# Kernel tuning notes

Hardware: AMD Instinct MI355X
Metric: run time of the kernel (lower is better)

## Reference

```python
import jax, jax.numpy as jnp
import numpy as np

N, D_IN, D_HID, D_OUT, E, STEPS = 50000, 64, 64, 32, 800000, 3


def setup_inputs() -> dict:
    key = jax.random.key(0)
    ks = jax.random.split(key, 8)
    x = jax.random.normal(ks[0], (N, D_IN), dtype=jnp.float32)
    edge_index = jax.random.randint(ks[1], (2, E), 0, N, dtype=jnp.int32)
    s1 = 1.0 / np.sqrt(2 * D_IN)
    s2 = 1.0 / np.sqrt(D_IN)
    s3 = 1.0 / np.sqrt(2 * D_HID)
    s4 = 1.0 / np.sqrt(D_HID)
    W_att1 = jax.random.uniform(ks[2], (2 * D_IN, 1), jnp.float32, -s1, s1)
    b_att1 = jax.random.uniform(ks[3], (1,), jnp.float32, -s1, s1)
    W_lin1 = jax.random.uniform(ks[4], (D_IN, D_HID), jnp.float32, -s2, s2)
    W_att2 = jax.random.uniform(ks[5], (2 * D_HID, 1), jnp.float32, -s3, s3)
    b_att2 = jax.random.uniform(ks[6], (1,), jnp.float32, -s3, s3)
    W_lin2 = jax.random.uniform(ks[7], (D_HID, D_OUT), jnp.float32, -s4, s4)
    return {"x": x, "edge_index": edge_index, "W_att1": W_att1, "b_att1": b_att1,
            "W_lin1": W_lin1, "W_att2": W_att2, "b_att2": b_att2, "W_lin2": W_lin2}


def _aggregate_mean(h, src, dst, n):
    # mean over incoming neighbors; nodes with no in-edges get 0 (clamped denom)
    feat_sum = jax.ops.segment_sum(h[src], dst, num_segments=n)
    deg = jax.ops.segment_sum(jnp.ones_like(src, dtype=h.dtype), dst, num_segments=n)
    return feat_sum / jnp.maximum(deg, 1.0)[:, None]


def _gcn_conv(x, src, dst, W_att, b_att, W_lin, n):
    h_src = x[src]                       # [E, d]
    h_dst = x[dst]                       # [E, d]
    score = jax.nn.leaky_relu(
        jnp.concatenate([h_src, h_dst], axis=-1) @ W_att + b_att)  # [E, 1]
    weighted = score * (h_src @ W_lin)   # [E, d_out]
    feats = jax.ops.segment_sum(weighted, dst, num_segments=n)
    att = jax.ops.segment_sum(jnp.abs(weighted), dst, num_segments=n)
    return feats, att


def reference(x, edge_index, W_att1, b_att1, W_lin1, W_att2, b_att2, W_lin2):
    src, dst = edge_index[0], edge_index[1]
    n = x.shape[0]
    # graphSmoothing positional encoding: stack of [x, mean^1(x), ..., mean^S(x)], then mean over steps
    h = x
    acc = x
    for _ in range(STEPS):
        h = _aggregate_mean(h, src, dst, n)
        acc = acc + h
    xs = acc / (STEPS + 1)
    h1, _att1 = _gcn_conv(xs, src, dst, W_att1, b_att1, W_lin1, n)
    h1 = jax.nn.relu(h1)  # dropout is identity in eval mode
    out, _att2 = _gcn_conv(h1, src, dst, W_att2, b_att2, W_lin2, n)
    # y=None -> loss_separation = loss_focus = 0
    return out
```

## Files before the change

kernel.cpp:

```cpp
#include <hip/hip_runtime.h>


typedef __attribute__((ext_vector_type(8))) _Float16 half8;
typedef __attribute__((ext_vector_type(4))) _Float16 half4v;
typedef __attribute__((ext_vector_type(2))) _Float16 half2v;

#define CHUNK 1024

#define UNPACK8(iraw, ss)                                                     \
    ss[0] = (iraw).x & 0xffffu; ss[1] = (iraw).x >> 16;                       \
    ss[2] = (iraw).y & 0xffffu; ss[3] = (iraw).y >> 16;                       \
    ss[4] = (iraw).z & 0xffffu; ss[5] = (iraw).z >> 16;                       \
    ss[6] = (iraw).w & 0xffffu; ss[7] = (iraw).w >> 16;

__global__ void binA_kernel(const int* __restrict__ src, const int* __restrict__ dst,
                            unsigned int* __restrict__ packed, int* __restrict__ offs,
                            const float* __restrict__ x, _Float16* __restrict__ x16,
                            int total8, int E) {
    __shared__ int cnt[256];
    __shared__ int pref[256];
    __shared__ int cur[256];
    __shared__ unsigned int stage[CHUNK];
    int t = threadIdx.x;
    int base = blockIdx.x * CHUNK;
    int len = E - base; if (len > CHUNK) len = CHUNK;
    cnt[t] = 0;
    __syncthreads();
    for (int i = t; i < len; i += 256) atomicAdd(&cnt[dst[base + i] >> 8], 1);
    __syncthreads();
    int v = cnt[t];
    pref[t] = v;
    __syncthreads();
    for (int off = 1; off < 256; off <<= 1) {
        int u = (t >= off) ? pref[t - off] : 0;
        __syncthreads();
        pref[t] += u;
        __syncthreads();
    }
    int excl = pref[t] - v;
    cur[t] = excl;
    offs[blockIdx.x * 257 + t] = excl;
    if (t == 255) offs[blockIdx.x * 257 + 256] = pref[255];
    __syncthreads();
    for (int i = t; i < len; i += 256) {
        int s = src[base + i], d = dst[base + i];
        int pos = atomicAdd(&cur[d >> 8], 1);
        stage[pos] = (unsigned int)s | ((unsigned int)d << 16);
    }
    __syncthreads();
    for (int i = t; i < len; i += 256) packed[base + i] = stage[i];
    for (int i = blockIdx.x * 256 + t; i < total8; i += gridDim.x * 256) {
        float4 v0 = ((const float4*)x)[2 * i];
        float4 v1 = ((const float4*)x)[2 * i + 1];
        half8 o;
        o[0] = (_Float16)v0.x; o[1] = (_Float16)v0.y; o[2] = (_Float16)v0.z; o[3] = (_Float16)v0.w;
        o[4] = (_Float16)v1.x; o[5] = (_Float16)v1.y; o[6] = (_Float16)v1.z; o[7] = (_Float16)v1.w;
        ((half8*)x16)[i] = o;
    }
}

__global__ void binB_kernel(const unsigned int* __restrict__ packed,
                            const int* __restrict__ offs,
                            int* __restrict__ deg,
                            unsigned short* __restrict__ src_idx,
                            int nChunks, int N) {
    __shared__ int cnt[256];
    int t = threadIdx.x;
    int p = blockIdx.x;
    if (t < 256) cnt[t] = 0;
    __syncthreads();
    size_t winBase = (size_t)p * 256 * 64;
    for (int c = t; c < nChunks; c += 512) {
        const int* oc = offs + c * 257;
        int o0 = oc[p], o1 = oc[p + 1];
        const unsigned int* pk = packed + (size_t)c * CHUNK;
        for (int i = o0; i < o1; ++i) {
            unsigned int pr = pk[i];
            int ln = (pr >> 16) & 255;
            int slot = atomicAdd(&cnt[ln], 1);
            if (slot < 64)
                src_idx[winBase + (size_t)ln * 64 + slot] = (unsigned short)(pr & 0xffffu);
        }
    }
    __syncthreads();
    if (t < 256) {
        int node = p * 256 + t;
        if (node < N) {
            int d = cnt[t];
            deg[node] = d < 64 ? d : 64;
        }
    }
}

__global__ void agg_mean8_kernel(const _Float16* __restrict__ h,
                                 const int* __restrict__ degp,
                                 const unsigned short* __restrict__ src_idx,
                                 _Float16* __restrict__ h_out, int N) {
    int wid = (blockIdx.x * blockDim.x + threadIdx.x) >> 6;
    int lane = threadIdx.x & 63;
    int node = wid * 2 + (lane >> 5);
    if (node >= N) return;
    int lane32 = lane & 31;
    int beg = node << 6;
    int j = lane32 >> 3, f = lane32 & 7;
    int base = beg + 8 * j;
    uint4 iraw0 = *(const uint4*)(src_idx + base);
    int dgr = degp[node];
    int end = beg + dgr;
    const uint4* rowp = (const uint4*)h;
    float acc[8];
    #pragma unroll
    for (int q = 0; q < 8; ++q) acc[q] = 0.f;
    if (base < end) {
        int ss[8];
        UNPACK8(iraw0, ss)
        #pragma unroll
        for (int k = 0; k < 8; ++k) {
            int e = base + k;
            int s = e < end ? ss[k] : ss[0];
            uint4 raw = rowp[(size_t)s * 8 + f];
            if (e >= end) { raw.x = 0u; raw.y = 0u; raw.z = 0u; raw.w = 0u; }
            half8 v = *(half8*)&raw;
            #pragma unroll
            for (int q = 0; q < 8; ++q) acc[q] += (float)v[q];
        }
    }
    int base1 = base + 32;
    if (base1 < end) {
        uint4 iraw1 = *(const uint4*)(src_idx + base1);
        int ss[8];
        UNPACK8(iraw1, ss)
        #pragma unroll
        for (int k = 0; k < 8; ++k) {
            int e = base1 + k;
            int s = e < end ? ss[k] : ss[0];
            uint4 raw = rowp[(size_t)s * 8 + f];
            if (e >= end) { raw.x = 0u; raw.y = 0u; raw.z = 0u; raw.w = 0u; }
            half8 v = *(half8*)&raw;
            #pragma unroll
            for (int q = 0; q < 8; ++q) acc[q] += (float)v[q];
        }
    }
    #pragma unroll
    for (int q = 0; q < 8; ++q) {
        acc[q] += __shfl_down(acc[q], 16, 64);
        acc[q] += __shfl_down(acc[q], 8, 64);
    }
    if (lane32 < 8) {
        float inv = dgr > 0 ? 1.f / (float)dgr : 0.f;
        half8 o;
        #pragma unroll
        for (int q = 0; q < 8; ++q) o[q] = (_Float16)(acc[q] * inv);
        *((half8*)h_out + (size_t)node * 8 + lane32) = o;
    }
}

__global__ void mean3_xf1_kernel(const _Float16* __restrict__ h ,
                                 const _Float16* __restrict__ x16,
                                 const _Float16* __restrict__ hA ,
                                 const int* __restrict__ degp,
                                 const unsigned short* __restrict__ src_idx,
                                 const float* __restrict__ W_lin1,
                                 const float* __restrict__ W_att1,
                                 _Float16* __restrict__ z1, float* __restrict__ a1,
                                 float* __restrict__ a2, int N) {
    __shared__ float Wl[64 * 64];
    __shared__ float Wa[128];
    __shared__ float rows[4][2][64];
    for (int i = threadIdx.x; i < 1024; i += 256)
        ((float4*)Wl)[i] = ((const float4*)W_lin1)[i];
    if (threadIdx.x < 128) Wa[threadIdx.x] = W_att1[threadIdx.x];
    __syncthreads();
    int w = threadIdx.x >> 6;
    int wid = (blockIdx.x * blockDim.x + threadIdx.x) >> 6;
    int lane = threadIdx.x & 63;
    int halfsel = lane >> 5;
    int node = wid * 2 + halfsel;
    if (node >= N) return;
    int lane32 = lane & 31;
    int beg = node << 6;
    int j = lane32 >> 3, f = lane32 & 7;
    int base = beg + 8 * j;
    uint4 iraw0 = *(const uint4*)(src_idx + base);
    int dgr = degp[node];
    int end = beg + dgr;
    const uint4* rowp = (const uint4*)h;
    float acc[8];
    #pragma unroll
    for (int q = 0; q < 8; ++q) acc[q] = 0.f;
    if (base < end) {
        int ss[8];
        UNPACK8(iraw0, ss)
        #pragma unroll
        for (int k = 0; k < 8; ++k) {
            int e = base + k;
            int s = e < end ? ss[k] : ss[0];
            uint4 raw = rowp[(size_t)s * 8 + f];
            if (e >= end) { raw.x = 0u; raw.y = 0u; raw.z = 0u; raw.w = 0u; }
            half8 v = *(half8*)&raw;
            #pragma unroll
            for (int q = 0; q < 8; ++q) acc[q] += (float)v[q];
        }
    }
    int base1 = base + 32;
    if (base1 < end) {
        uint4 iraw1 = *(const uint4*)(src_idx + base1);
        int ss[8];
        UNPACK8(iraw1, ss)
        #pragma unroll
        for (int k = 0; k < 8; ++k) {
            int e = base1 + k;
            int s = e < end ? ss[k] : ss[0];
            uint4 raw = rowp[(size_t)s * 8 + f];
            if (e >= end) { raw.x = 0u; raw.y = 0u; raw.z = 0u; raw.w = 0u; }
            half8 v = *(half8*)&raw;
            #pragma unroll
            for (int q = 0; q < 8; ++q) acc[q] += (float)v[q];
        }
    }
    #pragma unroll
    for (int q = 0; q < 8; ++q) {
        acc[q] += __shfl_down(acc[q], 16, 64);
        acc[q] += __shfl_down(acc[q], 8, 64);
    }
    float p1 = 0.f, p2 = 0.f;
    if (lane32 < 8) {
        float inv = dgr > 0 ? 1.f / (float)dgr : 0.f;
        half8 xv = *((const half8*)x16 + (size_t)node * 8 + f);
        half8 h1v = *((const half8*)hA + (size_t)node * 8 + f);
        half8 h2v = *((const half8*)h + (size_t)node * 8 + f);
        float xs[8];
        #pragma unroll
        for (int q = 0; q < 8; ++q) {
            xs[q] = ((float)xv[q] + (float)h1v[q] + (float)h2v[q] + acc[q] * inv) * 0.25f;
            p1 += xs[q] * Wa[f * 8 + q];
            p2 += xs[q] * Wa[64 + f * 8 + q];
        }
        *(float4*)&rows[w][halfsel][f * 8]     = make_float4(xs[0], xs[1], xs[2], xs[3]);
        *(float4*)&rows[w][halfsel][f * 8 + 4] = make_float4(xs[4], xs[5], xs[6], xs[7]);
    }
    p1 += __shfl_down(p1, 4, 64); p2 += __shfl_down(p2, 4, 64);
    p1 += __shfl_down(p1, 2, 64); p2 += __shfl_down(p2, 2, 64);
    p1 += __shfl_down(p1, 1, 64); p2 += __shfl_down(p2, 1, 64);
    if (lane32 == 0) { a1[node] = p1; a2[node] = p2; }
    float z0 = 0.f, zb = 0.f;
    const float4* myrow4 = (const float4*)rows[w][halfsel];
    #pragma unroll
    for (int k4 = 0; k4 < 16; ++k4) {
        float4 xk = myrow4[k4];
        float2 w0 = *(const float2*)&Wl[(4 * k4 + 0) * 64 + 2 * lane32];
        float2 w1 = *(const float2*)&Wl[(4 * k4 + 1) * 64 + 2 * lane32];
        float2 w2 = *(const float2*)&Wl[(4 * k4 + 2) * 64 + 2 * lane32];
        float2 w3 = *(const float2*)&Wl[(4 * k4 + 3) * 64 + 2 * lane32];
        z0 += xk.x * w0.x + xk.y * w1.x + xk.z * w2.x + xk.w * w3.x;
        zb += xk.x * w0.y + xk.y * w1.y + xk.z * w2.y + xk.w * w3.y;
    }
    half2v o2; o2.x = (_Float16)z0; o2.y = (_Float16)zb;
    *((half2v*)(z1 + (size_t)node * 64 + 2 * lane32)) = o2;
}

__global__ void conv64_xf2_kernel(const _Float16* __restrict__ z, const float* __restrict__ a1v,
                                  const float* __restrict__ a2v, const float* __restrict__ b_att,
                                  const int* __restrict__ degp,
                                  const unsigned short* __restrict__ src_idx,
                                  const float* __restrict__ W_lin2,
                                  const float* __restrict__ W_att2,
                                  _Float16* __restrict__ z2, float* __restrict__ a1o,
                                  float* __restrict__ a2o, int N) {
    __shared__ float Wl[64 * 32];
    __shared__ float Wa[128];
    __shared__ float rows[4][2][64];
    for (int i = threadIdx.x; i < 512; i += 256)
        ((float4*)Wl)[i] = ((const float4*)W_lin2)[i];
    if (threadIdx.x < 128) Wa[threadIdx.x] = W_att2[threadIdx.x];
    __syncthreads();
    int w = threadIdx.x >> 6;
    int wid = (blockIdx.x * blockDim.x + threadIdx.x) >> 6;
    int lane = threadIdx.x & 63;
    int halfsel = lane >> 5;
    int node = wid * 2 + halfsel;
    if (node >= N) return;
    int lane32 = lane & 31;
    int beg = node << 6;
    int j = lane32 >> 3, f = lane32 & 7;
    int base = beg + 8 * j;
    uint4 iraw0 = *(const uint4*)(src_idx + base);
    float ad = a2v[node] + b_att[0];
    int dgr = degp[node];
    int end = beg + dgr;
    const uint4* rowp = (const uint4*)z;
    float acc[8];
    #pragma unroll
    for (int q = 0; q < 8; ++q) acc[q] = 0.f;
    if (base < end) {
        int ss[8];
        UNPACK8(iraw0, ss)
        #pragma unroll
        for (int k = 0; k < 8; ++k) {
            int e = base + k;
            int s = e < end ? ss[k] : ss[0];
            float sc = a1v[s] + ad;
            sc = sc > 0.f ? sc : 0.01f * sc;
            uint4 raw = rowp[(size_t)s * 8 + f];
            if (e >= end) { raw.x = 0u; raw.y = 0u; raw.z = 0u; raw.w = 0u; }
            half8 v = *(half8*)&raw;
            #pragma unroll
            for (int q = 0; q < 8; ++q) acc[q] += sc * (float)v[q];
        }
    }
    int base1 = base + 32;
    if (base1 < end) {
        uint4 iraw1 = *(const uint4*)(src_idx + base1);
        int ss[8];
        UNPACK8(iraw1, ss)
        #pragma unroll
        for (int k = 0; k < 8; ++k) {
            int e = base1 + k;
            int s = e < end ? ss[k] : ss[0];
            float sc = a1v[s] + ad;
            sc = sc > 0.f ? sc : 0.01f * sc;
            uint4 raw = rowp[(size_t)s * 8 + f];
            if (e >= end) { raw.x = 0u; raw.y = 0u; raw.z = 0u; raw.w = 0u; }
            half8 v = *(half8*)&raw;
            #pragma unroll
            for (int q = 0; q < 8; ++q) acc[q] += sc * (float)v[q];
        }
    }
    #pragma unroll
    for (int q = 0; q < 8; ++q) {
        acc[q] += __shfl_down(acc[q], 16, 64);
        acc[q] += __shfl_down(acc[q], 8, 64);
    }
    float p1 = 0.f, p2 = 0.f;
    if (lane32 < 8) {
        float hreg[8];
        #pragma unroll
        for (int q = 0; q < 8; ++q) {
            hreg[q] = fmaxf(acc[q], 0.f);
            p1 += hreg[q] * Wa[f * 8 + q];
            p2 += hreg[q] * Wa[64 + f * 8 + q];
        }
        *(float4*)&rows[w][halfsel][f * 8]     = make_float4(hreg[0], hreg[1], hreg[2], hreg[3]);
        *(float4*)&rows[w][halfsel][f * 8 + 4] = make_float4(hreg[4], hreg[5], hreg[6], hreg[7]);
    }
    p1 += __shfl_down(p1, 4, 64); p2 += __shfl_down(p2, 4, 64);
    p1 += __shfl_down(p1, 2, 64); p2 += __shfl_down(p2, 2, 64);
    p1 += __shfl_down(p1, 1, 64); p2 += __shfl_down(p2, 1, 64);
    if (lane32 == 0) { a1o[node] = p1; a2o[node] = p2; }
    float zacc = 0.f;
    const float4* myrow4 = (const float4*)rows[w][halfsel];
    #pragma unroll
    for (int k4 = 0; k4 < 16; ++k4) {
        float4 hk = myrow4[k4];
        zacc += hk.x * Wl[(4 * k4 + 0) * 32 + lane32];
        zacc += hk.y * Wl[(4 * k4 + 1) * 32 + lane32];
        zacc += hk.z * Wl[(4 * k4 + 2) * 32 + lane32];
        zacc += hk.w * Wl[(4 * k4 + 3) * 32 + lane32];
    }
    z2[(size_t)node * 32 + lane32] = (_Float16)zacc;
}

__global__ void agg_conv32_kernel(const _Float16* __restrict__ z, const float* __restrict__ a1v,
                                  const float* __restrict__ a2v, const float* __restrict__ b_att,
                                  const int* __restrict__ degp,
                                  const unsigned short* __restrict__ src_idx,
                                  float* __restrict__ outp, int N) {
    int wid = (blockIdx.x * blockDim.x + threadIdx.x) >> 6;
    int lane = threadIdx.x & 63;
    int node = wid * 2 + (lane >> 5);
    if (node >= N) return;
    int lane32 = lane & 31;
    int beg = node << 6;
    int j = lane32 >> 3, f = lane32 & 7;
    int base = beg + 8 * j;
    uint4 iraw0 = *(const uint4*)(src_idx + base);
    float ad = a2v[node] + b_att[0];
    int dgr = degp[node];
    int end = beg + dgr;
    const uint2* rowp = (const uint2*)z;
    float ax = 0.f, ay = 0.f, az = 0.f, aw = 0.f;
    if (base < end) {
        int ss[8];
        UNPACK8(iraw0, ss)
        #pragma unroll
        for (int k = 0; k < 8; ++k) {
            int e = base + k;
            int s = e < end ? ss[k] : ss[0];
            float sc = a1v[s] + ad;
            sc = sc > 0.f ? sc : 0.01f * sc;
            uint2 raw = rowp[(size_t)s * 8 + f];
            if (e >= end) { raw.x = 0u; raw.y = 0u; }
            half4v v = *(half4v*)&raw;
            ax += sc * (float)v[0]; ay += sc * (float)v[1];
            az += sc * (float)v[2]; aw += sc * (float)v[3];
        }
    }
    int base1 = base + 32;
    if (base1 < end) {
        uint4 iraw1 = *(const uint4*)(src_idx + base1);
        int ss[8];
        UNPACK8(iraw1, ss)
        #pragma unroll
        for (int k = 0; k < 8; ++k) {
            int e = base1 + k;
            int s = e < end ? ss[k] : ss[0];
            float sc = a1v[s] + ad;
            sc = sc > 0.f ? sc : 0.01f * sc;
            uint2 raw = rowp[(size_t)s * 8 + f];
            if (e >= end) { raw.x = 0u; raw.y = 0u; }
            half4v v = *(half4v*)&raw;
            ax += sc * (float)v[0]; ay += sc * (float)v[1];
            az += sc * (float)v[2]; aw += sc * (float)v[3];
        }
    }
    ax += __shfl_down(ax, 16, 64); ay += __shfl_down(ay, 16, 64);
    az += __shfl_down(az, 16, 64); aw += __shfl_down(aw, 16, 64);
    ax += __shfl_down(ax, 8, 64);  ay += __shfl_down(ay, 8, 64);
    az += __shfl_down(az, 8, 64);  aw += __shfl_down(aw, 8, 64);
    if (lane32 < 8) {
        float4 o; o.x = ax; o.y = ay; o.z = az; o.w = aw;
        *((float4*)(outp + (size_t)node * 32) + lane32) = o;
    }
}

extern "C" void kernel_launch(void* const* d_in, const int* in_sizes, int n_in,
                              void* d_out, int out_size, void* d_ws, size_t ws_size,
                              hipStream_t stream) {
    const float* x      = (const float*)d_in[0];
    const int*   ei     = (const int*)d_in[1];
    const float* W_att1 = (const float*)d_in[2];
    const float* b_att1 = (const float*)d_in[3];
    const float* W_lin1 = (const float*)d_in[4];
    const float* W_att2 = (const float*)d_in[5];
    const float* b_att2 = (const float*)d_in[6];
    const float* W_lin2 = (const float*)d_in[7];
    float* out = (float*)d_out;

    int N = in_sizes[0] / 64;
    int E = in_sizes[1] / 2;
    const int* src = ei;
    const int* dst = ei + E;
    int nChunks = (E + CHUNK - 1) / CHUNK;
    int nPart   = (N + 255) >> 8;

    char* ws = (char*)d_ws;
    size_t off = 0;
    auto alloc = [&](size_t bytes) -> void* {
        void* p = ws + off;
        off += (bytes + 255) & ~(size_t)255;
        return p;
    };
    int*            deg     = (int*)alloc((size_t)N * 4);
    unsigned short* src_idx = (unsigned short*)alloc((size_t)nPart * 256 * 64 * 2);
    unsigned int*   packed  = (unsigned int*)alloc((size_t)nChunks * CHUNK * 4);
    int*            offs    = (int*)alloc((size_t)nChunks * 257 * 4);
    _Float16* x16 = (_Float16*)alloc((size_t)N * 64 * 2);
    _Float16* hA  = (_Float16*)alloc((size_t)N * 64 * 2);
    _Float16* hB  = (_Float16*)alloc((size_t)N * 64 * 2);
    _Float16* z1  = (_Float16*)alloc((size_t)N * 64 * 2);
    _Float16* z2  = (_Float16*)alloc((size_t)N * 32 * 2);
    float* a1  = (float*)alloc((size_t)N * 4);
    float* a2  = (float*)alloc((size_t)N * 4);
    float* a1b = (float*)alloc((size_t)N * 4);
    float* a2b = (float*)alloc((size_t)N * 4);

    const int tb = 256;
    int total8 = N * 8;

    binA_kernel<<<nChunks, 256, 0, stream>>>(src, dst, packed, offs, x, x16, total8, E);
    binB_kernel<<<nPart, 512, 0, stream>>>(packed, offs, deg, src_idx, nChunks, N);

    int gBlocks = (N + 7) / 8;
    agg_mean8_kernel<<<gBlocks, tb, 0, stream>>>(x16, deg, src_idx, hA, N);
    agg_mean8_kernel<<<gBlocks, tb, 0, stream>>>(hA,  deg, src_idx, hB, N);
    mean3_xf1_kernel<<<gBlocks, tb, 0, stream>>>(hB, x16, hA, deg, src_idx,
                                                 W_lin1, W_att1, z1, a1, a2, N);
    conv64_xf2_kernel<<<gBlocks, tb, 0, stream>>>(z1, a1, a2, b_att1, deg, src_idx,
                                                  W_lin2, W_att2, z2, a1b, a2b, N);
    agg_conv32_kernel<<<gBlocks, tb, 0, stream>>>(z2, a1b, a2b, b_att2, deg, src_idx,
                                                  out, N);
}
```

Baseline: 196.2 us.

## Fuse five aggregation stages into one cooperative persistent kernel with grid syncs

Replaces the five back-to-back per-stage kernel launches with a single cooperative persistent kernel. It grid-strides over node pairs and separates the stages with grid.sync(), reloading the shared-memory weights between conv stages. The stage bodies are factored into device functions shared with the fallback path. The aim is to remove launch gaps and tail effects between small kernels. In exchange, occupancy is capped by the cooperative grid size, and each grid barrier adds its own cost.

After: 476.4 us. +142.8%, slower.

```diff
diff --git a/kernel.cpp b/kernel.cpp
--- a/kernel.cpp
+++ b/kernel.cpp
@@ -1,4 +1,7 @@
 #include <hip/hip_runtime.h>
+#include <hip/hip_cooperative_groups.h>
+
+namespace cg = cooperative_groups;
 
 
 typedef __attribute__((ext_vector_type(8))) _Float16 half8;
@@ -92,6 +95,294 @@
     }
 }
 
+
+__device__ __forceinline__ void agg_mean_body(
+    const _Float16* __restrict__ h, _Float16* __restrict__ h_out,
+    const int* __restrict__ degp, const unsigned short* __restrict__ src_idx,
+    int node, int lane32, int j, int f) {
+    int beg = node << 6;
+    int base = beg + 8 * j;
+    uint4 iraw0 = *(const uint4*)(src_idx + base);
+    int dgr = degp[node];
+    int end = beg + dgr;
+    const uint4* rowp = (const uint4*)h;
+    float acc[8];
+    #pragma unroll
+    for (int q = 0; q < 8; ++q) acc[q] = 0.f;
+    if (base < end) {
+        int ss[8];
+        UNPACK8(iraw0, ss)
+        #pragma unroll
+        for (int k = 0; k < 8; ++k) {
+            int e = base + k;
+            int s = e < end ? ss[k] : ss[0];
+            uint4 raw = rowp[(size_t)s * 8 + f];
+            if (e >= end) { raw.x = 0u; raw.y = 0u; raw.z = 0u; raw.w = 0u; }
+            half8 v = *(half8*)&raw;
+            #pragma unroll
+            for (int q = 0; q < 8; ++q) acc[q] += (float)v[q];
+        }
+    }
+    int base1 = base + 32;
+    if (base1 < end) {
+        uint4 iraw1 = *(const uint4*)(src_idx + base1);
+        int ss[8];
+        UNPACK8(iraw1, ss)
+        #pragma unroll
+        for (int k = 0; k < 8; ++k) {
+            int e = base1 + k;
+            int s = e < end ? ss[k] : ss[0];
+            uint4 raw = rowp[(size_t)s * 8 + f];
+            if (e >= end) { raw.x = 0u; raw.y = 0u; raw.z = 0u; raw.w = 0u; }
+            half8 v = *(half8*)&raw;
+            #pragma unroll
+            for (int q = 0; q < 8; ++q) acc[q] += (float)v[q];
+        }
+    }
+    #pragma unroll
+    for (int q = 0; q < 8; ++q) {
+        acc[q] += __shfl_down(acc[q], 16, 64);
+        acc[q] += __shfl_down(acc[q], 8, 64);
+    }
+    if (lane32 < 8) {
+        float inv = dgr > 0 ? 1.f / (float)dgr : 0.f;
+        half8 o;
+        #pragma unroll
+        for (int q = 0; q < 8; ++q) o[q] = (_Float16)(acc[q] * inv);
+        *((half8*)h_out + (size_t)node * 8 + lane32) = o;
+    }
+}
+
+__device__ __forceinline__ void mean3_xf1_body(
+    const _Float16* __restrict__ h, const _Float16* __restrict__ x16,
+    const _Float16* __restrict__ hA,
+    const int* __restrict__ degp, const unsigned short* __restrict__ src_idx,
+    const float* Wl, const float* Wa, float* myrow,
+    _Float16* __restrict__ z1, float* __restrict__ a1, float* __restrict__ a2,
+    int node, int lane32, int j, int f) {
+    int beg = node << 6;
+    int base = beg + 8 * j;
+    uint4 iraw0 = *(const uint4*)(src_idx + base);
+    int dgr = degp[node];
+    int end = beg + dgr;
+    const uint4* rowp = (const uint4*)h;
+    float acc[8];
+    #pragma unroll
+    for (int q = 0; q < 8; ++q) acc[q] = 0.f;
+    if (base < end) {
+        int ss[8];
+        UNPACK8(iraw0, ss)
+        #pragma unroll
+        for (int k = 0; k < 8; ++k) {
+            int e = base + k;
+            int s = e < end ? ss[k] : ss[0];
+            uint4 raw = rowp[(size_t)s * 8 + f];
+            if (e >= end) { raw.x = 0u; raw.y = 0u; raw.z = 0u; raw.w = 0u; }
+            half8 v = *(half8*)&raw;
+            #pragma unroll
+            for (int q = 0; q < 8; ++q) acc[q] += (float)v[q];
+        }
+    }
+    int base1 = base + 32;
+    if (base1 < end) {
+        uint4 iraw1 = *(const uint4*)(src_idx + base1);
+        int ss[8];
+        UNPACK8(iraw1, ss)
+        #pragma unroll
+        for (int k = 0; k < 8; ++k) {
+            int e = base1 + k;
+            int s = e < end ? ss[k] : ss[0];
+            uint4 raw = rowp[(size_t)s * 8 + f];
+            if (e >= end) { raw.x = 0u; raw.y = 0u; raw.z = 0u; raw.w = 0u; }
+            half8 v = *(half8*)&raw;
+            #pragma unroll
+            for (int q = 0; q < 8; ++q) acc[q] += (float)v[q];
+        }
+    }
+    #pragma unroll
+    for (int q = 0; q < 8; ++q) {
+        acc[q] += __shfl_down(acc[q], 16, 64);
+        acc[q] += __shfl_down(acc[q], 8, 64);
+    }
+    float p1 = 0.f, p2 = 0.f;
+    if (lane32 < 8) {
+        float inv = dgr > 0 ? 1.f / (float)dgr : 0.f;
+        half8 xv = *((const half8*)x16 + (size_t)node * 8 + f);
+        half8 h1v = *((const half8*)hA + (size_t)node * 8 + f);
+        half8 h2v = *((const half8*)h + (size_t)node * 8 + f);
+        float xs[8];
+        #pragma unroll
+        for (int q = 0; q < 8; ++q) {
+            xs[q] = ((float)xv[q] + (float)h1v[q] + (float)h2v[q] + acc[q] * inv) * 0.25f;
+            p1 += xs[q] * Wa[f * 8 + q];
+            p2 += xs[q] * Wa[64 + f * 8 + q];
+        }
+        *(float4*)&myrow[f * 8]     = make_float4(xs[0], xs[1], xs[2], xs[3]);
+        *(float4*)&myrow[f * 8 + 4] = make_float4(xs[4], xs[5], xs[6], xs[7]);
+    }
+    p1 += __shfl_down(p1, 4, 64); p2 += __shfl_down(p2, 4, 64);
+    p1 += __shfl_down(p1, 2, 64); p2 += __shfl_down(p2, 2, 64);
+    p1 += __shfl_down(p1, 1, 64); p2 += __shfl_down(p2, 1, 64);
+    if (lane32 == 0) { a1[node] = p1; a2[node] = p2; }
+    float z0 = 0.f, zb = 0.f;
+    const float4* myrow4 = (const float4*)myrow;
+    #pragma unroll
+    for (int k4 = 0; k4 < 16; ++k4) {
+        float4 xk = myrow4[k4];
+        float2 w0 = *(const float2*)&Wl[(4 * k4 + 0) * 64 + 2 * lane32];
+        float2 w1 = *(const float2*)&Wl[(4 * k4 + 1) * 64 + 2 * lane32];
+        float2 w2 = *(const float2*)&Wl[(4 * k4 + 2) * 64 + 2 * lane32];
+        float2 w3 = *(const float2*)&Wl[(4 * k4 + 3) * 64 + 2 * lane32];
+        z0 += xk.x * w0.x + xk.y * w1.x + xk.z * w2.x + xk.w * w3.x;
+        zb += xk.x * w0.y + xk.y * w1.y + xk.z * w2.y + xk.w * w3.y;
+    }
+    half2v o2; o2.x = (_Float16)z0; o2.y = (_Float16)zb;
+    *((half2v*)(z1 + (size_t)node * 64 + 2 * lane32)) = o2;
+}
+
+__device__ __forceinline__ void conv64_xf2_body(
+    const _Float16* __restrict__ z, const float* __restrict__ a1v,
+    const float* __restrict__ a2v, const float* __restrict__ b_att,
+    const int* __restrict__ degp, const unsigned short* __restrict__ src_idx,
+    const float* Wl, const float* Wa, float* myrow,
+    _Float16* __restrict__ z2, float* __restrict__ a1o, float* __restrict__ a2o,
+    int node, int lane32, int j, int f) {
+    int beg = node << 6;
+    int base = beg + 8 * j;
+    uint4 iraw0 = *(const uint4*)(src_idx + base);
+    float ad = a2v[node] + b_att[0];
+    int dgr = degp[node];
+    int end = beg + dgr;
+    const uint4* rowp = (const uint4*)z;
+    float acc[8];
+    #pragma unroll
+    for (int q = 0; q < 8; ++q) acc[q] = 0.f;
+    if (base < end) {
+        int ss[8];
+        UNPACK8(iraw0, ss)
+        #pragma unroll
+        for (int k = 0; k < 8; ++k) {
+            int e = base + k;
+            int s = e < end ? ss[k] : ss[0];
+            float sc = a1v[s] + ad;
+            sc = sc > 0.f ? sc : 0.01f * sc;
+            uint4 raw = rowp[(size_t)s * 8 + f];
+            if (e >= end) { raw.x = 0u; raw.y = 0u; raw.z = 0u; raw.w = 0u; }
+            half8 v = *(half8*)&raw;
+            #pragma unroll
+            for (int q = 0; q < 8; ++q) acc[q] += sc * (float)v[q];
+        }
+    }
+    int base1 = base + 32;
+    if (base1 < end) {
+        uint4 iraw1 = *(const uint4*)(src_idx + base1);
+        int ss[8];
+        UNPACK8(iraw1, ss)
+        #pragma unroll
+        for (int k = 0; k < 8; ++k) {
+            int e = base1 + k;
+            int s = e < end ? ss[k] : ss[0];
+            float sc = a1v[s] + ad;
+            sc = sc > 0.f ? sc : 0.01f * sc;
+            uint4 raw = rowp[(size_t)s * 8 + f];
+            if (e >= end) { raw.x = 0u; raw.y = 0u; raw.z = 0u; raw.w = 0u; }
+            half8 v = *(half8*)&raw;
+            #pragma unroll
+            for (int q = 0; q < 8; ++q) acc[q] += sc * (float)v[q];
+        }
+    }
+    #pragma unroll
+    for (int q = 0; q < 8; ++q) {
+        acc[q] += __shfl_down(acc[q], 16, 64);
+        acc[q] += __shfl_down(acc[q], 8, 64);
+    }
+    float p1 = 0.f, p2 = 0.f;
+    if (lane32 < 8) {
+        float hreg[8];
+        #pragma unroll
+        for (int q = 0; q < 8; ++q) {
+            hreg[q] = fmaxf(acc[q], 0.f);
+            p1 += hreg[q] * Wa[f * 8 + q];
+            p2 += hreg[q] * Wa[64 + f * 8 + q];
+        }
+        *(float4*)&myrow[f * 8]     = make_float4(hreg[0], hreg[1], hreg[2], hreg[3]);
+        *(float4*)&myrow[f * 8 + 4] = make_float4(hreg[4], hreg[5], hreg[6], hreg[7]);
+    }
+    p1 += __shfl_down(p1, 4, 64); p2 += __shfl_down(p2, 4, 64);
+    p1 += __shfl_down(p1, 2, 64); p2 += __shfl_down(p2, 2, 64);
+    p1 += __shfl_down(p1, 1, 64); p2 += __shfl_down(p2, 1, 64);
+    if (lane32 == 0) { a1o[node] = p1; a2o[node] = p2; }
+    float zacc = 0.f;
+    const float4* myrow4 = (const float4*)myrow;
+    #pragma unroll
+    for (int k4 = 0; k4 < 16; ++k4) {
+        float4 hk = myrow4[k4];
+        zacc += hk.x * Wl[(4 * k4 + 0) * 32 + lane32];
+        zacc += hk.y * Wl[(4 * k4 + 1) * 32 + lane32];
+        zacc += hk.z * Wl[(4 * k4 + 2) * 32 + lane32];
+        zacc += hk.w * Wl[(4 * k4 + 3) * 32 + lane32];
+    }
+    z2[(size_t)node * 32 + lane32] = (_Float16)zacc;
+}
+
+__device__ __forceinline__ void agg_conv32_body(
+    const _Float16* __restrict__ z, const float* __restrict__ a1v,
+    const float* __restrict__ a2v, const float* __restrict__ b_att,
+    const int* __restrict__ degp, const unsigned short* __restrict__ src_idx,
+    float* __restrict__ outp, int node, int lane32, int j, int f) {
+    int beg = node << 6;
+    int base = beg + 8 * j;
+    uint4 iraw0 = *(const uint4*)(src_idx + base);
+    float ad = a2v[node] + b_att[0];
+    int dgr = degp[node];
+    int end = beg + dgr;
+    const uint2* rowp = (const uint2*)z;
+    float ax = 0.f, ay = 0.f, az = 0.f, aw = 0.f;
+    if (base < end) {
+        int ss[8];
+        UNPACK8(iraw0, ss)
+        #pragma unroll
+        for (int k = 0; k < 8; ++k) {
+            int e = base + k;
+            int s = e < end ? ss[k] : ss[0];
+            float sc = a1v[s] + ad;
+            sc = sc > 0.f ? sc : 0.01f * sc;
+            uint2 raw = rowp[(size_t)s * 8 + f];
+            if (e >= end) { raw.x = 0u; raw.y = 0u; }
+            half4v v = *(half4v*)&raw;
+            ax += sc * (float)v[0]; ay += sc * (float)v[1];
+            az += sc * (float)v[2]; aw += sc * (float)v[3];
+        }
+    }
+    int base1 = base + 32;
+    if (base1 < end) {
+        uint4 iraw1 = *(const uint4*)(src_idx + base1);
+        int ss[8];
+        UNPACK8(iraw1, ss)
+        #pragma unroll
+        for (int k = 0; k < 8; ++k) {
+            int e = base1 + k;
+            int s = e < end ? ss[k] : ss[0];
+            float sc = a1v[s] + ad;
+            sc = sc > 0.f ? sc : 0.01f * sc;
+            uint2 raw = rowp[(size_t)s * 8 + f];
+            if (e >= end) { raw.x = 0u; raw.y = 0u; }
+            half4v v = *(half4v*)&raw;
+            ax += sc * (float)v[0]; ay += sc * (float)v[1];
+            az += sc * (float)v[2]; aw += sc * (float)v[3];
+        }
+    }
+    ax += __shfl_down(ax, 16, 64); ay += __shfl_down(ay, 16, 64);
+    az += __shfl_down(az, 16, 64); aw += __shfl_down(aw, 16, 64);
+    ax += __shfl_down(ax, 8, 64);  ay += __shfl_down(ay, 8, 64);
+    az += __shfl_down(az, 8, 64);  aw += __shfl_down(aw, 8, 64);
+    if (lane32 < 8) {
+        float4 o; o.x = ax; o.y = ay; o.z = az; o.w = aw;
+        *((float4*)(outp + (size_t)node * 32) + lane32) = o;
+    }
+}
+
+
 __global__ void agg_mean8_kernel(const _Float16* __restrict__ h,
                                  const int* __restrict__ degp,
                                  const unsigned short* __restrict__ src_idx,
@@ -101,63 +392,12 @@
     int node = wid * 2 + (lane >> 5);
     if (node >= N) return;
     int lane32 = lane & 31;
-    int beg = node << 6;
-    int j = lane32 >> 3, f = lane32 & 7;
-    int base = beg + 8 * j;
-    uint4 iraw0 = *(const uint4*)(src_idx + base);
-    int dgr = degp[node];
-    int end = beg + dgr;
-    const uint4* rowp = (const uint4*)h;
-    float acc[8];
-    #pragma unroll
-    for (int q = 0; q < 8; ++q) acc[q] = 0.f;
-    if (base < end) {
-        int ss[8];
-        UNPACK8(iraw0, ss)
-        #pragma unroll
-        for (int k = 0; k < 8; ++k) {
-            int e = base + k;
-            int s = e < end ? ss[k] : ss[0];
-            uint4 raw = rowp[(size_t)s * 8 + f];
-            if (e >= end) { raw.x = 0u; raw.y = 0u; raw.z = 0u; raw.w = 0u; }
-            half8 v = *(half8*)&raw;
-            #pragma unroll
-            for (int q = 0; q < 8; ++q) acc[q] += (float)v[q];
-        }
-    }
-    int base1 = base + 32;
-    if (base1 < end) {
-        uint4 iraw1 = *(const uint4*)(src_idx + base1);
-        int ss[8];
-        UNPACK8(iraw1, ss)
-        #pragma unroll
-        for (int k = 0; k < 8; ++k) {
-            int e = base1 + k;
-            int s = e < end ? ss[k] : ss[0];
-            uint4 raw = rowp[(size_t)s * 8 + f];
-            if (e >= end) { raw.x = 0u; raw.y = 0u; raw.z = 0u; raw.w = 0u; }
-            half8 v = *(half8*)&raw;
-            #pragma unroll
-            for (int q = 0; q < 8; ++q) acc[q] += (float)v[q];
-        }
-    }
-    #pragma unroll
-    for (int q = 0; q < 8; ++q) {
-        acc[q] += __shfl_down(acc[q], 16, 64);
-        acc[q] += __shfl_down(acc[q], 8, 64);
-    }
-    if (lane32 < 8) {
-        float inv = dgr > 0 ? 1.f / (float)dgr : 0.f;
-        half8 o;
-        #pragma unroll
-        for (int q = 0; q < 8; ++q) o[q] = (_Float16)(acc[q] * inv);
-        *((half8*)h_out + (size_t)node * 8 + lane32) = o;
-    }
-}
-
-__global__ void mean3_xf1_kernel(const _Float16* __restrict__ h ,
+    agg_mean_body(h, h_out, degp, src_idx, node, lane32, lane32 >> 3, lane32 & 7);
+}
+
+__global__ void mean3_xf1_kernel(const _Float16* __restrict__ h,
                                  const _Float16* __restrict__ x16,
-                                 const _Float16* __restrict__ hA ,
+                                 const _Float16* __restrict__ hA,
                                  const int* __restrict__ degp,
                                  const unsigned short* __restrict__ src_idx,
                                  const float* __restrict__ W_lin1,
@@ -178,85 +418,8 @@
     int node = wid * 2 + halfsel;
     if (node >= N) return;
     int lane32 = lane & 31;
-    int beg = node << 6;
-    int j = lane32 >> 3, f = lane32 & 7;
-    int base = beg + 8 * j;
-    uint4 iraw0 = *(const uint4*)(src_idx + base);
-    int dgr = degp[node];
-    int end = beg + dgr;
-    const uint4* rowp = (const uint4*)h;
-    float acc[8];
-    #pragma unroll
-    for (int q = 0; q < 8; ++q) acc[q] = 0.f;
-    if (base < end) {
-        int ss[8];
-        UNPACK8(iraw0, ss)
-        #pragma unroll
-        for (int k = 0; k < 8; ++k) {
-            int e = base + k;
-            int s = e < end ? ss[k] : ss[0];
-            uint4 raw = rowp[(size_t)s * 8 + f];
-            if (e >= end) { raw.x = 0u; raw.y = 0u; raw.z = 0u; raw.w = 0u; }
-            half8 v = *(half8*)&raw;
-            #pragma unroll
-            for (int q = 0; q < 8; ++q) acc[q] += (float)v[q];
-        }
-    }
-    int base1 = base + 32;
-    if (base1 < end) {
-        uint4 iraw1 = *(const uint4*)(src_idx + base1);
-        int ss[8];
-        UNPACK8(iraw1, ss)
-        #pragma unroll
-        for (int k = 0; k < 8; ++k) {
-            int e = base1 + k;
-            int s = e < end ? ss[k] : ss[0];
-            uint4 raw = rowp[(size_t)s * 8 + f];
-            if (e >= end) { raw.x = 0u; raw.y = 0u; raw.z = 0u; raw.w = 0u; }
-            half8 v = *(half8*)&raw;
-            #pragma unroll
-            for (int q = 0; q < 8; ++q) acc[q] += (float)v[q];
-        }
-    }
-    #pragma unroll
-    for (int q = 0; q < 8; ++q) {
-        acc[q] += __shfl_down(acc[q], 16, 64);
-        acc[q] += __shfl_down(acc[q], 8, 64);
-    }
-    float p1 = 0.f, p2 = 0.f;
-    if (lane32 < 8) {
-        float inv = dgr > 0 ? 1.f / (float)dgr : 0.f;
-        half8 xv = *((const half8*)x16 + (size_t)node * 8 + f);
-        half8 h1v = *((const half8*)hA + (size_t)node * 8 + f);
-        half8 h2v = *((const half8*)h + (size_t)node * 8 + f);
-        float xs[8];
-        #pragma unroll
-        for (int q = 0; q < 8; ++q) {
-            xs[q] = ((float)xv[q] + (float)h1v[q] + (float)h2v[q] + acc[q] * inv) * 0.25f;
-            p1 += xs[q] * Wa[f * 8 + q];
-            p2 += xs[q] * Wa[64 + f * 8 + q];
-        }
-        *(float4*)&rows[w][halfsel][f * 8]     = make_float4(xs[0], xs[1], xs[2], xs[3]);
-        *(float4*)&rows[w][halfsel][f * 8 + 4] = make_float4(xs[4], xs[5], xs[6], xs[7]);
-    }
-    p1 += __shfl_down(p1, 4, 64); p2 += __shfl_down(p2, 4, 64);
-    p1 += __shfl_down(p1, 2, 64); p2 += __shfl_down(p2, 2, 64);
-    p1 += __shfl_down(p1, 1, 64); p2 += __shfl_down(p2, 1, 64);
-    if (lane32 == 0) { a1[node] = p1; a2[node] = p2; }
-    float z0 = 0.f, zb = 0.f;
-    const float4* myrow4 = (const float4*)rows[w][halfsel];
-    #pragma unroll
-    for (int k4 = 0; k4 < 16; ++k4) {
-        float4 xk = myrow4[k4];
-        float2 w0 = *(const float2*)&Wl[(4 * k4 + 0) * 64 + 2 * lane32];
-        float2 w1 = *(const float2*)&Wl[(4 * k4 + 1) * 64 + 2 * lane32];
-        float2 w2 = *(const float2*)&Wl[(4 * k4 + 2) * 64 + 2 * lane32];
-        float2 w3 = *(const float2*)&Wl[(4 * k4 + 3) * 64 + 2 * lane32];
-        z0 += xk.x * w0.x + xk.y * w1.x + xk.z * w2.x + xk.w * w3.x;
-        zb += xk.x * w0.y + xk.y * w1.y + xk.z * w2.y + xk.w * w3.y;
-    }
-    half2v o2; o2.x = (_Float16)z0; o2.y = (_Float16)zb;
-    *((half2v*)(z1 + (size_t)node * 64 + 2 * lane32)) = o2;
+    mean3_xf1_body(h, x16, hA, degp, src_idx, Wl, Wa, rows[w][halfsel],
+                   z1, a1, a2, node, lane32, lane32 >> 3, lane32 & 7);
 }
 
 __global__ void conv64_xf2_kernel(const _Float16* __restrict__ z, const float* __restrict__ a1v,
@@ -281,83 +444,8 @@
     int node = wid * 2 + halfsel;
     if (node >= N) return;
     int lane32 = lane & 31;
-    int beg = node << 6;
-    int j = lane32 >> 3, f = lane32 & 7;
-    int base = beg + 8 * j;
-    uint4 iraw0 = *(const uint4*)(src_idx + base);
-    float ad = a2v[node] + b_att[0];
-    int dgr = degp[node];
-    int end = beg + dgr;
-    const uint4* rowp = (const uint4*)z;
-    float acc[8];
-    #pragma unroll
-    for (int q = 0; q < 8; ++q) acc[q] = 0.f;
-    if (base < end) {
-        int ss[8];
-        UNPACK8(iraw0, ss)
-        #pragma unroll
-        for (int k = 0; k < 8; ++k) {
-            int e = base + k;
-            int s = e < end ? ss[k] : ss[0];
-            float sc = a1v[s] + ad;
-            sc = sc > 0.f ? sc : 0.01f * sc;
-            uint4 raw = rowp[(size_t)s * 8 + f];
-            if (e >= end) { raw.x = 0u; raw.y = 0u; raw.z = 0u; raw.w = 0u; }
-            half8 v = *(half8*)&raw;
-            #pragma unroll
-            for (int q = 0; q < 8; ++q) acc[q] += sc * (float)v[q];
-        }
-    }
-    int base1 = base + 32;
-    if (base1 < end) {
-        uint4 iraw1 = *(const uint4*)(src_idx + base1);
-        int ss[8];
-        UNPACK8(iraw1, ss)
-        #pragma unroll
-        for (int k = 0; k < 8; ++k) {
-            int e = base1 + k;
-            int s = e < end ? ss[k] : ss[0];
-            float sc = a1v[s] + ad;
-            sc = sc > 0.f ? sc : 0.01f * sc;
-            uint4 raw = rowp[(size_t)s * 8 + f];
-            if (e >= end) { raw.x = 0u; raw.y = 0u; raw.z = 0u; raw.w = 0u; }
-            half8 v = *(half8*)&raw;
-            #pragma unroll
-            for (int q = 0; q < 8; ++q) acc[q] += sc * (float)v[q];
-        }
-    }
-    #pragma unroll
-    for (int q = 0; q < 8; ++q) {
-        acc[q] += __shfl_down(acc[q], 16, 64);
-        acc[q] += __shfl_down(acc[q], 8, 64);
-    }
-    float p1 = 0.f, p2 = 0.f;
-    if (lane32 < 8) {
-        float hreg[8];
-        #pragma unroll
-        for (int q = 0; q < 8; ++q) {
-            hreg[q] = fmaxf(acc[q], 0.f);
-            p1 += hreg[q] * Wa[f * 8 + q];
-            p2 += hreg[q] * Wa[64 + f * 8 + q];
-        }
-        *(float4*)&rows[w][halfsel][f * 8]     = make_float4(hreg[0], hreg[1], hreg[2], hreg[3]);
-        *(float4*)&rows[w][halfsel][f * 8 + 4] = make_float4(hreg[4], hreg[5], hreg[6], hreg[7]);
-    }
-    p1 += __shfl_down(p1, 4, 64); p2 += __shfl_down(p2, 4, 64);
-    p1 += __shfl_down(p1, 2, 64); p2 += __shfl_down(p2, 2, 64);
-    p1 += __shfl_down(p1, 1, 64); p2 += __shfl_down(p2, 1, 64);
-    if (lane32 == 0) { a1o[node] = p1; a2o[node] = p2; }
-    float zacc = 0.f;
-    const float4* myrow4 = (const float4*)rows[w][halfsel];
-    #pragma unroll
-    for (int k4 = 0; k4 < 16; ++k4) {
-        float4 hk = myrow4[k4];
-        zacc += hk.x * Wl[(4 * k4 + 0) * 32 + lane32];
-        zacc += hk.y * Wl[(4 * k4 + 1) * 32 + lane32];
-        zacc += hk.z * Wl[(4 * k4 + 2) * 32 + lane32];
-        zacc += hk.w * Wl[(4 * k4 + 3) * 32 + lane32];
-    }
-    z2[(size_t)node * 32 + lane32] = (_Float16)zacc;
+    conv64_xf2_body(z, a1v, a2v, b_att, degp, src_idx, Wl, Wa, rows[w][halfsel],
+                    z2, a1o, a2o, node, lane32, lane32 >> 3, lane32 & 7);
 }
 
 __global__ void agg_conv32_kernel(const _Float16* __restrict__ z, const float* __restrict__ a1v,
@@ -370,56 +458,68 @@
     int node = wid * 2 + (lane >> 5);
     if (node >= N) return;
     int lane32 = lane & 31;
-    int beg = node << 6;
+    agg_conv32_body(z, a1v, a2v, b_att, degp, src_idx, outp,
+                    node, lane32, lane32 >> 3, lane32 & 7);
+}
+
+__global__ void fused5_kernel(
+    const _Float16* __restrict__ x16, _Float16* __restrict__ hA,
+    _Float16* __restrict__ hB,
+    const int* __restrict__ degp, const unsigned short* __restrict__ src_idx,
+    const float* __restrict__ W_lin1, const float* __restrict__ W_att1,
+    const float* __restrict__ W_lin2, const float* __restrict__ W_att2,
+    const float* __restrict__ b_att1, const float* __restrict__ b_att2,
+    _Float16* __restrict__ z1, _Float16* __restrict__ z2,
+    float* __restrict__ a1, float* __restrict__ a2,
+    float* __restrict__ a1b, float* __restrict__ a2b,
+    float* __restrict__ outp, int N) {
+    cg::grid_group grid = cg::this_grid();
+    __shared__ float Wl[64 * 64];
+    __shared__ float Wa[128];
+    __shared__ float rows[4][2][64];
+    int t = threadIdx.x;
+    int w = t >> 6;
+    int lane = t & 63;
+    int halfsel = lane >> 5;
+    int lane32 = lane & 31;
     int j = lane32 >> 3, f = lane32 & 7;
-    int base = beg + 8 * j;
-    uint4 iraw0 = *(const uint4*)(src_idx + base);
-    float ad = a2v[node] + b_att[0];
-    int dgr = degp[node];
-    int end = beg + dgr;
-    const uint2* rowp = (const uint2*)z;
-    float ax = 0.f, ay = 0.f, az = 0.f, aw = 0.f;
-    if (base < end) {
-        int ss[8];
-        UNPACK8(iraw0, ss)
-        #pragma unroll
-        for (int k = 0; k < 8; ++k) {
-            int e = base + k;
-            int s = e < end ? ss[k] : ss[0];
-            float sc = a1v[s] + ad;
-            sc = sc > 0.f ? sc : 0.01f * sc;
-            uint2 raw = rowp[(size_t)s * 8 + f];
-            if (e >= end) { raw.x = 0u; raw.y = 0u; }
-            half4v v = *(half4v*)&raw;
-            ax += sc * (float)v[0]; ay += sc * (float)v[1];
-            az += sc * (float)v[2]; aw += sc * (float)v[3];
-        }
-    }
-    int base1 = base + 32;
-    if (base1 < end) {
-        uint4 iraw1 = *(const uint4*)(src_idx + base1);
-        int ss[8];
-        UNPACK8(iraw1, ss)
-        #pragma unroll
-        for (int k = 0; k < 8; ++k) {
-            int e = base1 + k;
-            int s = e < end ? ss[k] : ss[0];
-            float sc = a1v[s] + ad;
-            sc = sc > 0.f ? sc : 0.01f * sc;
-            uint2 raw = rowp[(size_t)s * 8 + f];
-            if (e >= end) { raw.x = 0u; raw.y = 0u; }
-            half4v v = *(half4v*)&raw;
-            ax += sc * (float)v[0]; ay += sc * (float)v[1];
-            az += sc * (float)v[2]; aw += sc * (float)v[3];
-        }
-    }
-    ax += __shfl_down(ax, 16, 64); ay += __shfl_down(ay, 16, 64);
-    az += __shfl_down(az, 16, 64); aw += __shfl_down(aw, 16, 64);
-    ax += __shfl_down(ax, 8, 64);  ay += __shfl_down(ay, 8, 64);
-    az += __shfl_down(az, 8, 64);  aw += __shfl_down(aw, 8, 64);
-    if (lane32 < 8) {
-        float4 o; o.x = ax; o.y = ay; o.z = az; o.w = aw;
-        *((float4*)(outp + (size_t)node * 32) + lane32) = o;
+    float* myrow = rows[w][halfsel];
+    int waveId = (blockIdx.x * blockDim.x + t) >> 6;
+    int totWaves = (gridDim.x * blockDim.x) >> 6;
+    int nPairs = (N + 1) >> 1;
+
+    for (int np = waveId; np < nPairs; np += totWaves) {
+        int node = np * 2 + halfsel;
+        if (node < N) agg_mean_body(x16, hA, degp, src_idx, node, lane32, j, f);
+    }
+    grid.sync();
+    for (int np = waveId; np < nPairs; np += totWaves) {
+        int node = np * 2 + halfsel;
+        if (node < N) agg_mean_body(hA, hB, degp, src_idx, node, lane32, j, f);
+    }
+    grid.sync();
+    for (int i = t; i < 1024; i += 256) ((float4*)Wl)[i] = ((const float4*)W_lin1)[i];
+    if (t < 128) Wa[t] = W_att1[t];
+    __syncthreads();
+    for (int np = waveId; np < nPairs; np += totWaves) {
+        int node = np * 2 + halfsel;
+        if (node < N) mean3_xf1_body(hB, x16, hA, degp, src_idx, Wl, Wa, myrow,
+                                     z1, a1, a2, node, lane32, j, f);
+    }
+    grid.sync();
+    for (int i = t; i < 512; i += 256) ((float4*)Wl)[i] = ((const float4*)W_lin2)[i];
+    if (t < 128) Wa[t] = W_att2[t];
+    __syncthreads();
+    for (int np = waveId; np < nPairs; np += totWaves) {
+        int node = np * 2 + halfsel;
+        if (node < N) conv64_xf2_body(z1, a1, a2, b_att1, degp, src_idx, Wl, Wa, myrow,
+                                      z2, a1b, a2b, node, lane32, j, f);
+    }
+    grid.sync();
+    for (int np = waveId; np < nPairs; np += totWaves) {
+        int node = np * 2 + halfsel;
+        if (node < N) agg_conv32_body(z2, a1b, a2b, b_att2, degp, src_idx, outp,
+                                      node, lane32, j, f);
     }
 }
 
@@ -470,13 +570,36 @@
     binA_kernel<<<nChunks, 256, 0, stream>>>(src, dst, packed, offs, x, x16, total8, E);
     binB_kernel<<<nPart, 512, 0, stream>>>(packed, offs, deg, src_idx, nChunks, N);
 
+    static int coopGrid = -2;
+    if (coopGrid == -2) {
+        int perCU = 0;
+        hipError_t e = hipOccupancyMaxActiveBlocksPerMultiprocessor(
+            &perCU, fused5_kernel, tb, 0);
+        coopGrid = (e == hipSuccess && perCU > 0) ? perCU * 256 : 1024;
+    }
     int gBlocks = (N + 7) / 8;
-    agg_mean8_kernel<<<gBlocks, tb, 0, stream>>>(x16, deg, src_idx, hA, N);
-    agg_mean8_kernel<<<gBlocks, tb, 0, stream>>>(hA,  deg, src_idx, hB, N);
-    mean3_xf1_kernel<<<gBlocks, tb, 0, stream>>>(hB, x16, hA, deg, src_idx,
-                                                 W_lin1, W_att1, z1, a1, a2, N);
-    conv64_xf2_kernel<<<gBlocks, tb, 0, stream>>>(z1, a1, a2, b_att1, deg, src_idx,
-                                                  W_lin2, W_att2, z2, a1b, a2b, N);
-    agg_conv32_kernel<<<gBlocks, tb, 0, stream>>>(z2, a1b, a2b, b_att2, deg, src_idx,
-                                                  out, N);
-}
+    bool coopOK = false;
+    if (coopGrid > 0) {
+        int grid5 = coopGrid < gBlocks ? coopGrid : gBlocks;
+        void* kargs[] = {
+            (void*)&x16, (void*)&hA, (void*)&hB, (void*)&deg, (void*)&src_idx,
+            (void*)&W_lin1, (void*)&W_att1, (void*)&W_lin2, (void*)&W_att2,
+            (void*)&b_att1, (void*)&b_att2, (void*)&z1, (void*)&z2,
+            (void*)&a1, (void*)&a2, (void*)&a1b, (void*)&a2b,
+            (void*)&out, (void*)&N };
+        hipError_t e = hipLaunchCooperativeKernel(fused5_kernel, dim3(grid5), dim3(tb),
+                                                  kargs, 0u, stream);
+        if (e == hipSuccess) coopOK = true;
+        else coopGrid = 0;
+    }
+    if (!coopOK) {
+        agg_mean8_kernel<<<gBlocks, tb, 0, stream>>>(x16, deg, src_idx, hA, N);
+        agg_mean8_kernel<<<gBlocks, tb, 0, stream>>>(hA,  deg, src_idx, hB, N);
+        mean3_xf1_kernel<<<gBlocks, tb, 0, stream>>>(hB, x16, hA, deg, src_idx,
+                                                     W_lin1, W_att1, z1, a1, a2, N);
+        conv64_xf2_kernel<<<gBlocks, tb, 0, stream>>>(z1, a1, a2, b_att1, deg, src_idx,
+                                                      W_lin2, W_att2, z2, a1b, a2b, N);
+        agg_conv32_kernel<<<gBlocks, tb, 0, stream>>>(z2, a1b, a2b, b_att2, deg, src_idx,
+                                                      out, N);
+    }
+}
```
